# Kernel optimization log

Hardware: AMD Instinct MI355X
Metric: run time of the kernel (lower is better)

Reference implementation:

```python
import jax, jax.numpy as jnp
import numpy as np

PAD = 1
STRIDE = (1, 1)
TEMPERATURE = 1.0


def setup_inputs() -> dict:
    key = jax.random.key(0)
    ks = jax.random.split(key, 5)
    x = jax.random.normal(ks[0], (16, 256, 56, 56), dtype=jnp.float32)
    kernels = jax.random.normal(ks[1], (8, 256, 256, 3, 3), dtype=jnp.float32)
    w1 = jax.random.normal(ks[2], (256, 64), dtype=jnp.float32) * 0.0625
    b1 = jnp.zeros((64,), dtype=jnp.float32)
    w2 = jax.random.normal(ks[3], (64, 8), dtype=jnp.float32) * 0.125
    b2 = jnp.zeros((8,), dtype=jnp.float32)
    return {"x": x, "kernels": kernels, "w1": w1, "b1": b1, "w2": w2, "b2": b2}


def _forward(x, kernels, w1, b1, w2, b2):
    # Attention: global average pool -> MLP -> softmax over kernels
    pooled = jnp.mean(x, axis=(2, 3))                      # [B, C]
    h = jax.nn.relu(pooled @ w1 + b1)                      # [B, H]
    scores = h @ w2 + b2                                   # [B, K]
    alphas = jax.nn.softmax(scores / TEMPERATURE, axis=-1) # [B, K]

    # Per-sample mixed kernels: [B, O, I, kh, kw]
    weighted = jnp.einsum('bk,koihw->boihw', alphas, kernels)

    # Per-sample conv2d (groups=1), vectorized over batch
    def conv_one(xi, wi):
        return jax.lax.conv_general_dilated(
            xi[None], wi, STRIDE, [(PAD, PAD), (PAD, PAD)],
            dimension_numbers=('NCHW', 'OIHW', 'NCHW'))[0]

    return jax.vmap(conv_one)(x, weighted)                 # [B, O, H, W]


def reference(x, kernels, w1, b1, w2, b2):
    return _forward(x, kernels, w1, b1, w2, b2)
```

## Files before the change

kernel.cpp:

```cpp
#include <hip/hip_runtime.h>
#include <hip/hip_bf16.h>
#include <stdint.h>

typedef __attribute__((ext_vector_type(8))) short bf16x8;
typedef __attribute__((ext_vector_type(4))) float f32x4;

#define BATCH 16
#define CH    256
#define HW    56
#define HWHW  3136
#define NK    8

#define XPT_BYTES   30408704ul
#define WK_BYTES    18874368ul
#define POOL_BYTES  16384ul
#define ALPHA_BYTES 512ul

__device__ __forceinline__ void gl_lds16(const void* g, void* l) {
    __builtin_amdgcn_global_load_lds((const __attribute__((address_space(1))) uint32_t*)g,
                                     (__attribute__((address_space(3))) uint32_t*)l, 16, 0, 0);
}

__device__ __forceinline__ float bf16bits_to_f32(short h) {
    return __uint_as_float(((uint32_t)(uint16_t)h) << 16);
}

__global__ void __launch_bounds__(256, 2)
xpose_pool_kernel(const float* __restrict__ x, __hip_bfloat16* __restrict__ xp,
                  float* __restrict__ pooled) {
    __shared__ short tile[2 * 56 * 256];
    const int tid = threadIdx.x;
    const int ys  = blockIdx.x;
    const int b   = blockIdx.y;
    const int y0  = ys * 2;

    const float* xb = x + (size_t)b * CH * HWHW + (size_t)y0 * HW;
    for (int it = 0; it < 28; ++it) {
        int idx = it * 256 + tid;
        int ch  = idx / 28;
        int xi  = idx - ch * 28;
        int r   = xi / 14;
        int x4  = (xi - r * 14) * 4;
        const float4 v = *(const float4*)(xb + (size_t)ch * HWHW + r * HW + x4);
        const float* vf = (const float*)&v;
#pragma unroll
        for (int j = 0; j < 4; ++j) {
            __hip_bfloat16 h = __float2bfloat16(vf[j]);
            tile[(r * 56 + x4 + j) * 256 + (ch ^ (((x4 & 7) | j) << 3))] = *(const short*)&h;
        }
    }
    __syncthreads();

    {
        float s = 0.f;
        const int ch = tid;
        for (int r = 0; r < 2; ++r)
            for (int xx = 0; xx < 56; ++xx)
                s += bf16bits_to_f32(tile[(r * 56 + xx) * 256 + (ch ^ ((xx & 7) << 3))]);
        atomicAdd(&pooled[b * 256 + ch], s * (1.0f / 3136.0f));
    }

    __hip_bfloat16* dst0 = xp + ((size_t)(b * 58 + y0 + 1) * 64 + 1) * 256;
    for (int it = 0; it < 14; ++it) {
        int idx = it * 256 + tid;
        int ch0 = (idx & 31) * 8;
        int pos = idx >> 5;
        int r = pos / 56, xx = pos - (pos / 56) * 56;
        bf16x8 vv = *(const bf16x8*)&tile[(r * 56 + xx) * 256 + (ch0 ^ ((xx & 7) << 3))];
        *(bf16x8*)(dst0 + ((size_t)(r * 64 + xx)) * 256 + ch0) = vv;
    }

    bf16x8 z = {};
    if (tid < 128) {
        int r   = tid >> 6;
        int c2  = (tid >> 5) & 1;
        int ch0 = (tid & 31) * 8;
        *(bf16x8*)(xp + ((size_t)(b * 58 + y0 + 1 + r) * 64 + (c2 ? 57 : 0)) * 256 + ch0) = z;
    }
    if (ys == 0 || ys == 27) {
        int p = (ys == 0) ? 0 : 57;
        __hip_bfloat16* rowp = xp + (size_t)(b * 58 + p) * 64 * 256;
        for (int it = tid; it < 2048; it += 256)
            *(bf16x8*)(rowp + (size_t)it * 8) = z;
    }
}

__global__ void __launch_bounds__(256)
mlp_kernel(const float* __restrict__ pooled,
           const float* __restrict__ w1, const float* __restrict__ b1,
           const float* __restrict__ w2, const float* __restrict__ b2,
           float* __restrict__ alphas) {
    const int b = blockIdx.x;
    __shared__ float pl[256];
    __shared__ float hp[4][64];
    __shared__ float h[64];
    __shared__ float sc[8];
    int t = threadIdx.x;
    pl[t] = pooled[b * 256 + t];
    __syncthreads();
    int j = t & 63, part = t >> 6;
    float s = 0.f;
    const float* w1p = w1 + part * 64 * 64 + j;
#pragma unroll 8
    for (int c = 0; c < 64; ++c) s += pl[part * 64 + c] * w1p[c * 64];
    hp[part][j] = s;
    __syncthreads();
    if (t < 64) h[t] = fmaxf(hp[0][t] + hp[1][t] + hp[2][t] + hp[3][t] + b1[t], 0.f);
    __syncthreads();
    if (t < 8) {
        float acc = b2[t];
#pragma unroll 8
        for (int jj = 0; jj < 64; ++jj) acc += h[jj] * w2[jj * 8 + t];
        sc[t] = acc;
    }
    __syncthreads();
    if (t == 0) {
        float m = sc[0];
#pragma unroll
        for (int k = 1; k < 8; ++k) m = fmaxf(m, sc[k]);
        float ssum = 0.f, e[8];
#pragma unroll
        for (int k = 0; k < 8; ++k) { e[k] = expf(sc[k] - m); ssum += e[k]; }
        float inv = 1.0f / ssum;
#pragma unroll
        for (int k = 0; k < 8; ++k) alphas[b * 8 + k] = e[k] * inv;
    }
}

__global__ void wmix_kernel(const float* __restrict__ kern, const float* __restrict__ alphas,
                            __hip_bfloat16* __restrict__ wk) {
    __shared__ float al[16][8];
    int t = threadIdx.x;
    if (t < 128) al[t >> 3][t & 7] = alphas[t];
    __syncthreads();
    const int o = blockIdx.x, i = t;
    const int idx = o * 256 + i;
    const size_t ibase = (size_t)((i >> 5) * 16384 + ((o >> 4)) * 1024 + (o & 15) * 64 +
                                  ((i >> 3) & 3) * 16 + (i & 7) * 2);
    float kv[8][9];
    const float* kp = kern + (size_t)idx * 9;
#pragma unroll
    for (int k = 0; k < 8; ++k)
#pragma unroll
        for (int q = 0; q < 9; ++q) kv[k][q] = kp[(size_t)k * 589824 + q];
    char* wkb = (char*)wk;
#pragma unroll 1
    for (int b = 0; b < 16; ++b) {
#pragma unroll
        for (int q = 0; q < 9; ++q) {
            float acc = 0.f;
#pragma unroll
            for (int k = 0; k < 8; ++k) acc += al[b][k] * kv[k][q];
            __hip_bfloat16 h = __float2bfloat16(acc);
            *(short*)(wkb + (size_t)(b * 9 + q) * 131072 + ibase) = *(const short*)&h;
        }
    }
}

__global__ void __launch_bounds__(256, 2)
conv_kernel(const __hip_bfloat16* __restrict__ xpT, const __hip_bfloat16* __restrict__ wk,
            float* __restrict__ out) {
    __shared__ short lds_x[2][6 * 64 * 32];

    const int tid   = threadIdx.x;
    const int lane  = tid & 63;
    const int g     = lane >> 4;
    const int l15   = lane & 15;
    const int w     = tid >> 6;
    const int wm    = w >> 1;
    const int wn    = w & 1;
    const int w64   = tid & ~63;

    const int flat  = blockIdx.x;
    const int swzid = (flat & 7) * 56 + (flat >> 3);
    const int b     = swzid / 28;
    const int rem   = swzid - b * 28;
    const int mtile = rem & 1;
    const int y0    = (rem >> 1) * 4;

    int cellb[7], cc[7], rr[7];
#pragma unroll
    for (int fn = 0; fn < 7; ++fn) {
        int n = wn * 112 + fn * 16 + l15;
        int r = n / 56, c = n % 56;
        rr[fn] = r; cc[fn] = c;
        cellb[fn] = r * 64 + c;
    }

    f32x4 acc[4][7];
#pragma unroll
    for (int fm = 0; fm < 4; ++fm)
#pragma unroll
        for (int fn = 0; fn < 7; ++fn) acc[fm][fn] = (f32x4){0.f, 0.f, 0.f, 0.f};

    const size_t xb = ((size_t)b * 58 + y0) * 64 * 256;
    const char* wkb = (const char*)wk + (size_t)(b * 9) * 131072 +
                      (size_t)((mtile * 8 + wm * 4) * 1024 + l15 * 64 + g * 16);

#define STAGE_X(CI, BUF)                                                            \
    do {                                                                            \
        _Pragma("unroll")                                                           \
        for (int it = 0; it < 6; ++it) {                                            \
            int idx = it * 256 + tid;                                               \
            int sg  = idx & 3, cell = idx >> 2;                                     \
            int c = cell & 63;                                                      \
            int h = sg ^ ((c >> 1) & 3);                                            \
            const __hip_bfloat16* src = xpT + xb + (size_t)cell * 256 + (CI) * 32 + h * 8; \
            gl_lds16(src, (char*)lds_x[BUF] + (it * 256 + w64) * 16);               \
        }                                                                           \
    } while (0)

#define STEP(KK)                                                                    \
    do {                                                                            \
        bf16x8 af[4];                                                               \
        _Pragma("unroll")                                                           \
        for (int fm = 0; fm < 4; ++fm)                                              \
            af[fm] = *(const bf16x8*)(wkb + (size_t)((KK) * 131072 + ci * 16384 + fm * 1024)); \
        const int kh = (KK) / 3, kw = (KK) % 3;                                     \
        _Pragma("unroll")                                                           \
        for (int fn = 0; fn < 7; ++fn) {                                            \
            int cell = cellb[fn] + kh * 64 + kw;                                    \
            int slot = g ^ (((cc[fn] + kw) >> 1) & 3);                              \
            bf16x8 bfv = *(const bf16x8*)(xlds + cell * 64 + (slot << 4));          \
            _Pragma("unroll")                                                       \
            for (int fm = 0; fm < 4; ++fm)                                          \
                acc[fm][fn] = __builtin_amdgcn_mfma_f32_16x16x32_bf16(af[fm], bfv, acc[fm][fn], 0, 0, 0); \
        }                                                                           \
    } while (0)

    STAGE_X(0, 0);
    __syncthreads();

#pragma unroll 1
    for (int ci = 0; ci < 8; ++ci) {
        const char* xlds = (const char*)lds_x[ci & 1];
        if (ci < 7) STAGE_X(ci + 1, (ci & 1) ^ 1);
        STEP(0); STEP(1); STEP(2);
        STEP(3); STEP(4); STEP(5);
        STEP(6); STEP(7); STEP(8);
        if (ci < 7) __syncthreads();
    }

    const int mbase = mtile * 128 + wm * 64;
#pragma unroll
    for (int fm = 0; fm < 4; ++fm)
#pragma unroll
        for (int fn = 0; fn < 7; ++fn) {
            int o = mbase + fm * 16 + 4 * g;
            float* op = out + (((size_t)b * 256 + o) * 56 + (y0 + rr[fn])) * 56 + cc[fn];
#pragma unroll
            for (int r = 0; r < 4; ++r) op[(size_t)r * HWHW] = acc[fm][fn][r];
        }
#undef STAGE_X
#undef STEP
}

extern "C" void kernel_launch(void* const* d_in, const int* in_sizes, int n_in,
                              void* d_out, int out_size, void* d_ws, size_t ws_size,
                              hipStream_t stream) {
    const float* x    = (const float*)d_in[0];
    const float* kern = (const float*)d_in[1];
    const float* w1   = (const float*)d_in[2];
    const float* b1   = (const float*)d_in[3];
    const float* w2   = (const float*)d_in[4];
    const float* b2   = (const float*)d_in[5];
    float* out = (float*)d_out;

    char* wsp = (char*)d_ws;
    __hip_bfloat16* xpT    = (__hip_bfloat16*)wsp;
    __hip_bfloat16* wkbuf  = (__hip_bfloat16*)(wsp + XPT_BYTES);
    float*          pooled = (float*)(wsp + XPT_BYTES + WK_BYTES);
    float*          alphas = (float*)(wsp + XPT_BYTES + WK_BYTES + POOL_BYTES);

    hipMemsetAsync(pooled, 0, POOL_BYTES, stream);

    xpose_pool_kernel<<<dim3(28, 16), dim3(256), 0, stream>>>(x, xpT, pooled);
    mlp_kernel<<<dim3(16), dim3(256), 0, stream>>>(pooled, w1, b1, w2, b2, alphas);
    wmix_kernel<<<dim3(256), dim3(256), 0, stream>>>(kern, alphas, wkbuf);
    conv_kernel<<<dim3(448), dim3(256), 0, stream>>>(xpT, wkbuf, out);
}
```

Baseline: 244.1 us.

## Double-buffer A/B fragment registers across conv taps and raise MFMA priority

Splits each 3x3 tap step into separate fragment loads and MFMA blocks, using two register sets so the loads for the next tap are issued while the current tap's MFMAs run. MFMA sections are wrapped in s_setprio to favour matrix issue. Launch bounds drop to one block per SIMD-group to give the extra fragment registers room, and the row index is recomputed at store time instead of being held in registers. This trades occupancy, two blocks per CU down to possibly one, for better instruction-level overlap within each wave.

```diff
diff --git a/kernel.cpp b/kernel.cpp
--- a/kernel.cpp
+++ b/kernel.cpp
@@ -157,7 +157,7 @@
     }
 }
 
-__global__ void __launch_bounds__(256, 2)
+__global__ void __launch_bounds__(256, 1)
 conv_kernel(const __hip_bfloat16* __restrict__ xpT, const __hip_bfloat16* __restrict__ wk,
             float* __restrict__ out) {
     __shared__ short lds_x[2][6 * 64 * 32];
@@ -178,12 +178,12 @@
     const int mtile = rem & 1;
     const int y0    = (rem >> 1) * 4;
 
-    int cellb[7], cc[7], rr[7];
+    int cellb[7], cc[7];
 #pragma unroll
     for (int fn = 0; fn < 7; ++fn) {
         int n = wn * 112 + fn * 16 + l15;
         int r = n / 56, c = n % 56;
-        rr[fn] = r; cc[fn] = c;
+        cc[fn] = c;
         cellb[fn] = r * 64 + c;
     }
 
@@ -210,22 +210,33 @@
         }                                                                           \
     } while (0)
 
-#define STEP(KK)                                                                    \
+#define LOADA(KK, AR)                                                               \
     do {                                                                            \
-        bf16x8 af[4];                                                               \
         _Pragma("unroll")                                                           \
         for (int fm = 0; fm < 4; ++fm)                                              \
-            af[fm] = *(const bf16x8*)(wkb + (size_t)((KK) * 131072 + ci * 16384 + fm * 1024)); \
+            AR[fm] = *(const bf16x8*)(wkb + (size_t)((KK) * 131072 + ci * 16384 + fm * 1024)); \
+    } while (0)
+
+#define LOADB(KK, BR)                                                               \
+    do {                                                                            \
         const int kh = (KK) / 3, kw = (KK) % 3;                                     \
         _Pragma("unroll")                                                           \
         for (int fn = 0; fn < 7; ++fn) {                                            \
             int cell = cellb[fn] + kh * 64 + kw;                                    \
             int slot = g ^ (((cc[fn] + kw) >> 1) & 3);                              \
-            bf16x8 bfv = *(const bf16x8*)(xlds + cell * 64 + (slot << 4));          \
+            BR[fn] = *(const bf16x8*)(xlds + cell * 64 + (slot << 4));              \
+        }                                                                           \
+    } while (0)
+
+#define MM(AR, BR)                                                                  \
+    do {                                                                            \
+        __builtin_amdgcn_s_setprio(1);                                              \
+        _Pragma("unroll")                                                           \
+        for (int fn = 0; fn < 7; ++fn)                                              \
             _Pragma("unroll")                                                       \
             for (int fm = 0; fm < 4; ++fm)                                          \
-                acc[fm][fn] = __builtin_amdgcn_mfma_f32_16x16x32_bf16(af[fm], bfv, acc[fm][fn], 0, 0, 0); \
-        }                                                                           \
+                acc[fm][fn] = __builtin_amdgcn_mfma_f32_16x16x32_bf16(AR[fm], BR[fn], acc[fm][fn], 0, 0, 0); \
+        __builtin_amdgcn_s_setprio(0);                                              \
     } while (0)
 
     STAGE_X(0, 0);
@@ -234,10 +245,19 @@
 #pragma unroll 1
     for (int ci = 0; ci < 8; ++ci) {
         const char* xlds = (const char*)lds_x[ci & 1];
+        bf16x8 afA[4], afB[4], bfA[7], bfB[7];
+        LOADA(0, afA); LOADB(0, bfA);
         if (ci < 7) STAGE_X(ci + 1, (ci & 1) ^ 1);
-        STEP(0); STEP(1); STEP(2);
-        STEP(3); STEP(4); STEP(5);
-        STEP(6); STEP(7); STEP(8);
+        LOADA(1, afB); LOADB(1, bfB);
+        MM(afA, bfA);
+        LOADA(2, afA); LOADB(2, bfA); MM(afB, bfB);
+        LOADA(3, afB); LOADB(3, bfB); MM(afA, bfA);
+        LOADA(4, afA); LOADB(4, bfA); MM(afB, bfB);
+        LOADA(5, afB); LOADB(5, bfB); MM(afA, bfA);
+        LOADA(6, afA); LOADB(6, bfA); MM(afB, bfB);
+        LOADA(7, afB); LOADB(7, bfB); MM(afA, bfA);
+        LOADA(8, afA); LOADB(8, bfA); MM(afB, bfB);
+        MM(afA, bfA);
         if (ci < 7) __syncthreads();
     }
 
@@ -246,13 +266,17 @@
     for (int fm = 0; fm < 4; ++fm)
 #pragma unroll
         for (int fn = 0; fn < 7; ++fn) {
+            int n = wn * 112 + fn * 16 + l15;
+            int r = n / 56, c = n - (n / 56) * 56;
             int o = mbase + fm * 16 + 4 * g;
-            float* op = out + (((size_t)b * 256 + o) * 56 + (y0 + rr[fn])) * 56 + cc[fn];
-#pragma unroll
-            for (int r = 0; r < 4; ++r) op[(size_t)r * HWHW] = acc[fm][fn][r];
+            float* op = out + (((size_t)b * 256 + o) * 56 + (y0 + r)) * 56 + c;
+#pragma unroll
+            for (int q = 0; q < 4; ++q) op[(size_t)q * HWHW] = acc[fm][fn][q];
         }
 #undef STAGE_X
-#undef STEP
+#undef LOADA
+#undef LOADB
+#undef MM
 }
 
 extern "C" void kernel_launch(void* const* d_in, const int* in_sizes, int n_in,
```

After: 236.8 us. 1.03x faster.
